# Kernel tuning notes

Hardware: AMD Instinct MI355X
Metric: run time of the kernel (lower is better)

The kernel has to match this reference:

```python
import jax, jax.numpy as jnp
import numpy as np

N_NODES = 20000
N_EDGES = 320000
NS = 16      # input scalar channels (0e)
NVH = 16     # hidden vector channels (1o)
STEPS = 3
BLOCKS = 2
SQRT3 = 3.0 ** 0.5  # component-normalized Y1


def _tp(xs, xv, ys, yv):
    """Tensor product of (0e,1o) features with (0e,1o) attrs, keeping 0e and 1o outputs.
    xs:[n,a] xv:[n,b,3] ys:[n,c] yv:[n,d,3] -> ts:[n,a*c+b*d], tv:[n,a*d+b*c,3]"""
    n = xs.shape[0]
    ss = jnp.einsum('na,nc->nac', xs, ys).reshape(n, -1)          # 0e x 0e -> 0e
    vv = jnp.einsum('nbi,ndi->nbd', xv, yv).reshape(n, -1)        # 1o . 1o -> 0e
    ts = jnp.concatenate([ss, vv], axis=-1)
    sv = jnp.einsum('na,ndi->nadi', xs, yv).reshape(n, -1, 3)     # 0e x 1o -> 1o
    vs = jnp.einsum('nbi,nc->nbci', xv, ys).reshape(n, -1, 3)     # 1o x 0e -> 1o
    tv = jnp.concatenate([sv, vs], axis=1)
    return ts, tv


def _tplg(xs, xv, ys, yv, Ws, bs, Wv, out_v):
    """TensorProductLinearGate: tensor product -> Linear -> gate (sigmoid gates on vectors, gelu on scalars)."""
    ts, tv = _tp(xs, xv, ys, yv)
    s = ts @ Ws + bs                                  # [n, out_v (gates) + out_s]
    v = jnp.einsum('npi,pq->nqi', tv, Wv)             # [n, out_v, 3]
    gates = jax.nn.sigmoid(s[:, :out_v])
    feat = jax.nn.gelu(s[:, out_v:])
    return feat, v * gates[:, :, None]


def _seg_mean(x, idx, n):
    s = jax.ops.segment_sum(x, idx, num_segments=n)
    cnt = jax.ops.segment_sum(jnp.ones((idx.shape[0],), x.dtype), idx, num_segments=n)
    return s / jnp.maximum(cnt, 1.0).reshape((n,) + (1,) * (x.ndim - 1))


def setup_inputs() -> dict:
    key = jax.random.key(0)
    ks = jax.random.split(key, 20)

    def w(k, shape):
        return jax.random.normal(k, shape, jnp.float32) / np.sqrt(shape[-2]).astype(np.float32)

    return {
        'node_scalars': jax.random.normal(ks[0], (N_NODES, NS), jnp.float32),
        'node_pos': jax.random.normal(ks[1], (N_NODES, 1, 3), jnp.float32),
        'senders': jax.random.randint(ks[2], (N_EDGES,), 0, N_NODES, jnp.int32),
        'receivers': jax.random.randint(ks[3], (N_EDGES,), 0, N_NODES, jnp.int32),
        'eWs0': w(ks[4], (STEPS, 34, 32)),
        'ebs0': jnp.zeros((STEPS, 32), jnp.float32),
        'eWv0': w(ks[5], (STEPS, 34, NVH)),
        'eWs1': w(ks[6], (STEPS, 32, 32)),
        'ebs1': jnp.zeros((STEPS, 32), jnp.float32),
        'eWv1': w(ks[7], (STEPS, 32, NVH)),
        'nWs': w(ks[8], (STEPS, BLOCKS, 289, 17)),
        'nbs': jnp.zeros((STEPS, BLOCKS, 17), jnp.float32),
        'nWv': w(ks[9], (STEPS, BLOCKS, 289, 1)),
        'fWs': w(ks[10], (STEPS, NS, NS)),
        'fbs': jnp.zeros((STEPS, NS), jnp.float32),
        'fWv': w(ks[11], (STEPS, 1, 1)),
    }


def reference(node_scalars, node_pos, senders, receivers, eWs0, ebs0, eWv0,
              eWs1, ebs1, eWv1, nWs, nbs, nWv, fWs, fbs, fWv):
    s, v = node_scalars, node_pos                      # [N,16], [N,1,3]
    N = s.shape[0]
    E = senders.shape[0]
    inv = 1.0 / (E - 1)                                # normalize_messages
    for t in range(STEPS):
        # --- edge update ---
        r = v[senders, 0] - v[receivers, 0]            # r_ij = x_i - x_j
        rhat = r / (jnp.linalg.norm(r, axis=-1, keepdims=True) + 1e-8)
        a_s = jnp.ones((E, 1), s.dtype)                # Y0 (component norm)
        a_v = (SQRT3 * rhat)[:, None, :]               # Y1 (component norm)
        xs = jnp.concatenate([s[senders], s[receivers]], axis=-1)
        xv = jnp.concatenate([v[senders], v[receivers]], axis=1)
        ms, mv = _tplg(xs, xv, a_s, a_v, eWs0[t], ebs0[t], eWv0[t], NVH)
        ms, mv = _tplg(ms, mv, a_s, a_v, eWs1[t], ebs1[t], eWv1[t], NVH)
        # --- aggregate (segment mean to receivers) + message normalization ---
        ys = jnp.concatenate([_seg_mean(ms, receivers, N), _seg_mean(a_s, receivers, N)], axis=-1) * inv
        yv = jnp.concatenate([_seg_mean(mv, receivers, N), _seg_mean(a_v, receivers, N)], axis=1) * inv
        # --- node update ---
        ns_, nv_ = s, v
        for b in range(BLOCKS):
            ns_, nv_ = _tplg(ns_, nv_, ys, yv, nWs[t, b], nbs[t, b], nWv[t, b], 1)
        # --- Linear back to irreps_in + residual ---
        s = s + ns_ @ fWs[t] + fbs[t]
        v = v + jnp.einsum('npi,pq->nqi', nv_, fWv[t])
    return jnp.concatenate([s, v.reshape(N, 3)], axis=-1)  # [N, 19]
```

## Files before the change

kernel.cpp:

```cpp
#include <hip/hip_runtime.h>

#define N_NODES 20000
#define N_EDGES 320000
#define CH 68

__device__ __forceinline__ float sigm(float x) { return 1.0f / (1.0f + __expf(-x)); }
__device__ __forceinline__ float gelu(float x) {
    return x * sigm(1.5957691216057308f * (x + 0.044715f * x * x * x));
}

__global__ void init_kernel(const float* __restrict__ s0, const float* __restrict__ p0,
                            float* __restrict__ s, float4* __restrict__ v4,
                            float* __restrict__ cnt) {
    int idx = blockIdx.x * 256 + threadIdx.x;
    if (idx < N_NODES * 16) s[idx] = s0[idx];
    if (idx < N_NODES) {
        v4[idx] = make_float4(p0[idx * 3], p0[idx * 3 + 1], p0[idx * 3 + 2], 0.f);
        cnt[idx] = 0.f;
    }
}

__global__ void count_kernel(const int* __restrict__ rcv, float* __restrict__ cnt) {
    int e = blockIdx.x * 256 + threadIdx.x;
    if (e < N_EDGES) unsafeAtomicAdd(&cnt[rcv[e]], 1.0f);
}

__global__ __launch_bounds__(1024) void scan_kernel(const float* __restrict__ cnt,
                                                    int* __restrict__ offs,
                                                    int* __restrict__ cursor) {
    __shared__ int sdata[1024];
    const int t = threadIdx.x;
    const int base = t * 20;
    int local[20];
    int sum = 0;
#pragma unroll
    for (int k = 0; k < 20; k++) {
        const int n = base + k;
        const int c = (n < N_NODES) ? (int)cnt[n] : 0;
        local[k] = sum;
        sum += c;
    }
    sdata[t] = sum;
    __syncthreads();
    for (int d = 1; d < 1024; d <<= 1) {
        const int v = (t >= d) ? sdata[t - d] : 0;
        __syncthreads();
        sdata[t] += v;
        __syncthreads();
    }
    const int pre = (t == 0) ? 0 : sdata[t - 1];
#pragma unroll
    for (int k = 0; k < 20; k++) {
        const int n = base + k;
        if (n < N_NODES) {
            offs[n] = pre + local[k];
            cursor[n] = 0;
        }
    }
}

__global__ void scatter_kernel(const int* __restrict__ rcv, const int* __restrict__ offs,
                               int* __restrict__ cursor, int* __restrict__ perm) {
    int e = blockIdx.x * 256 + threadIdx.x;
    if (e < N_EDGES) {
        const int n = rcv[e];
        const int slot = offs[n] + atomicAdd(&cursor[n], 1);
        perm[slot] = e;
    }
}

__global__ __launch_bounds__(256) void edge_compute_kernel(
    const float4* __restrict__ s4, const float4* __restrict__ v4,
    const int* __restrict__ snd, const int* __restrict__ rcv,
    const int* __restrict__ perm,
    const float* __restrict__ Ws0, const float* __restrict__ bs0, const float* __restrict__ Wv0,
    const float* __restrict__ Ws1, const float* __restrict__ bs1, const float* __restrict__ Wv1,
    float* __restrict__ msg) {
    __shared__ float lW[3168];
    const int tid = threadIdx.x;
    {
        for (int idx = tid; idx < 1088; idx += 256) lW[idx] = Ws0[idx];
        for (int idx = tid; idx < 544; idx += 256) lW[1088 + idx] = Wv0[idx];
        for (int idx = tid; idx < 1024; idx += 256) lW[1632 + idx] = Ws1[idx];
        for (int idx = tid; idx < 512; idx += 256) lW[2656 + idx] = Wv1[idx];
    }
    __syncthreads();
    const float* __restrict__ lWs0 = lW;
    const float* __restrict__ lWv0 = lW + 1088;
    const float* __restrict__ lWs1 = lW + 1632;
    const float* __restrict__ lWv1 = lW + 2656;

    const int e = blockIdx.x * 256 + tid;
    const int eid = perm[e];
    const int i = snd[eid], j = rcv[eid];

    const float4 vi4 = v4[i], vj4 = v4[j];
    const float vi0 = vi4.x, vi1 = vi4.y, vi2 = vi4.z;
    const float vj0 = vj4.x, vj1 = vj4.y, vj2 = vj4.z;
    const float r0 = vi0 - vj0, r1 = vi1 - vj1, r2 = vi2 - vj2;
    const float nrm = sqrtf(r0 * r0 + r1 * r1 + r2 * r2);
    const float scl = 1.7320508075688772f / (nrm + 1e-8f);
    const float a0 = r0 * scl, a1 = r1 * scl, a2 = r2 * scl;

    float xs[32];
    {
        float4 A = s4[i * 4 + 0], B = s4[i * 4 + 1], C = s4[i * 4 + 2], D = s4[i * 4 + 3];
        xs[0] = A.x; xs[1] = A.y; xs[2] = A.z; xs[3] = A.w;
        xs[4] = B.x; xs[5] = B.y; xs[6] = B.z; xs[7] = B.w;
        xs[8] = C.x; xs[9] = C.y; xs[10] = C.z; xs[11] = C.w;
        xs[12] = D.x; xs[13] = D.y; xs[14] = D.z; xs[15] = D.w;
        A = s4[j * 4 + 0]; B = s4[j * 4 + 1]; C = s4[j * 4 + 2]; D = s4[j * 4 + 3];
        xs[16] = A.x; xs[17] = A.y; xs[18] = A.z; xs[19] = A.w;
        xs[20] = B.x; xs[21] = B.y; xs[22] = B.z; xs[23] = B.w;
        xs[24] = C.x; xs[25] = C.y; xs[26] = C.z; xs[27] = C.w;
        xs[28] = D.x; xs[29] = D.y; xs[30] = D.z; xs[31] = D.w;
    }
    const float di = vi0 * a0 + vi1 * a1 + vi2 * a2;
    const float dj = vj0 * a0 + vj1 * a1 + vj2 * a2;

    float sl[32];
#pragma unroll
    for (int o = 0; o < 32; o++) sl[o] = bs0[o] + di * lWs0[32 * 32 + o] + dj * lWs0[33 * 32 + o];
#pragma unroll
    for (int p = 0; p < 32; p++) {
        const float x = xs[p];
#pragma unroll
        for (int o = 0; o < 32; o++) sl[o] += x * lWs0[p * 32 + o];
    }
    float al[16];
#pragma unroll
    for (int q = 0; q < 16; q++) al[q] = 0.f;
#pragma unroll
    for (int p = 0; p < 32; p++) {
        const float x = xs[p];
#pragma unroll
        for (int q = 0; q < 16; q++) al[q] += x * lWv0[p * 16 + q];
    }
    float ms[16], mv0[16], mv1[16], mv2[16];
#pragma unroll
    for (int q = 0; q < 16; q++) {
        const float g = sigm(sl[q]);
        const float w32 = lWv0[32 * 16 + q], w33 = lWv0[33 * 16 + q];
        mv0[q] = (al[q] * a0 + w32 * vi0 + w33 * vj0) * g;
        mv1[q] = (al[q] * a1 + w32 * vi1 + w33 * vj1) * g;
        mv2[q] = (al[q] * a2 + w32 * vi2 + w33 * vj2) * g;
    }
#pragma unroll
    for (int p = 0; p < 16; p++) ms[p] = gelu(sl[16 + p]);

    float sl2[32];
#pragma unroll
    for (int o = 0; o < 32; o++) sl2[o] = bs1[o];
#pragma unroll
    for (int p = 0; p < 16; p++) {
        const float x = ms[p];
#pragma unroll
        for (int o = 0; o < 32; o++) sl2[o] += x * lWs1[p * 32 + o];
    }
#pragma unroll
    for (int q = 0; q < 16; q++) {
        const float x = mv0[q] * a0 + mv1[q] * a1 + mv2[q] * a2;
#pragma unroll
        for (int o = 0; o < 32; o++) sl2[o] += x * lWs1[(16 + q) * 32 + o];
    }

    float4* mrow = (float4*)(msg + (size_t)e * CH);
    mrow[0] = make_float4(gelu(sl2[16]), gelu(sl2[17]), gelu(sl2[18]), gelu(sl2[19]));
    mrow[1] = make_float4(gelu(sl2[20]), gelu(sl2[21]), gelu(sl2[22]), gelu(sl2[23]));
    mrow[2] = make_float4(gelu(sl2[24]), gelu(sl2[25]), gelu(sl2[26]), gelu(sl2[27]));
    mrow[3] = make_float4(gelu(sl2[28]), gelu(sl2[29]), gelu(sl2[30]), gelu(sl2[31]));
#pragma unroll
    for (int qg = 0; qg < 4; qg++) {
        float t[12];
#pragma unroll
        for (int qq = 0; qq < 4; qq++) {
            const int q = qg * 4 + qq;
            const float g = sigm(sl2[q]);
            float be = 0.f;
#pragma unroll
            for (int p = 0; p < 16; p++) be += ms[p] * lWv1[p * 16 + q];
            float u0 = be * a0, u1 = be * a1, u2 = be * a2;
#pragma unroll
            for (int p = 0; p < 16; p++) {
                const float w = lWv1[(16 + p) * 16 + q];
                u0 += mv0[p] * w; u1 += mv1[p] * w; u2 += mv2[p] * w;
            }
            t[qq * 3 + 0] = u0 * g;
            t[qq * 3 + 1] = u1 * g;
            t[qq * 3 + 2] = u2 * g;
        }
        mrow[4 + qg * 3 + 0] = make_float4(t[0], t[1], t[2], t[3]);
        mrow[4 + qg * 3 + 1] = make_float4(t[4], t[5], t[6], t[7]);
        mrow[4 + qg * 3 + 2] = make_float4(t[8], t[9], t[10], t[11]);
    }
    mrow[16] = make_float4(a0, a1, a2, 0.f);
}

__global__ __launch_bounds__(256) void agg_kernel(const float* __restrict__ msg,
                                                  const float* __restrict__ cnt,
                                                  const int* __restrict__ offs,
                                                  float* __restrict__ agg) {
    const int id = blockIdx.x * 256 + threadIdx.x;
    if (id >= N_NODES * CH) return;
    const int n = id / CH;
    const int c = id - n * CH;
    const int deg = (int)cnt[n];
    const float* p = msg + (size_t)offs[n] * CH + c;
    float acc = 0.f;
    int r = 0;
    for (; r + 4 <= deg; r += 4) {
        acc += p[(size_t)(r + 0) * CH] + p[(size_t)(r + 1) * CH] +
               p[(size_t)(r + 2) * CH] + p[(size_t)(r + 3) * CH];
    }
    for (; r < deg; r++) acc += p[(size_t)r * CH];
    agg[id] = acc;
}

__global__ __launch_bounds__(256, 2) void node_kernel(
    float* __restrict__ s, float4* __restrict__ v4,
    float* __restrict__ agg, const float* __restrict__ cntb,
    const float* __restrict__ nWs, const float* __restrict__ nbs, const float* __restrict__ nWv,
    const float* __restrict__ fWs, const float* __restrict__ fbs, const float* __restrict__ fWv,
    float* __restrict__ out) {
    __shared__ float nsl[64 * 17];
    __shared__ float part[21 * 256];
    const int tid = threadIdx.x;
    const int lane = tid & 63;
    const int w = tid >> 6;
    const int n0 = blockIdx.x * 64 + lane;
    const bool valid = n0 < N_NODES;
    const int n = valid ? n0 : 0;
    const float inv = 1.0f / 319999.0f;
    const float cnt = cntb[n];
    const float f = inv / fmaxf(cnt, 1.0f);
    float* ag = agg + n * CH;
    const int c0 = w * 4;
    const bool w3 = (w == 3);

    float yso[4];
#pragma unroll
    for (int k = 0; k < 4; k++) yso[k] = ag[c0 + k] * f;
    const float ys16 = cnt * f;
    float yvo[4][3];
#pragma unroll
    for (int k = 0; k < 4; k++) {
        const int d = c0 + k;
        yvo[k][0] = ag[16 + d * 3 + 0] * f;
        yvo[k][1] = ag[16 + d * 3 + 1] * f;
        yvo[k][2] = ag[16 + d * 3 + 2] * f;
    }
    float yv16[3] = {ag[64] * f, ag[65] * f, ag[66] * f};
    const float4 nvv = v4[n];
    float nv0 = nvv.x, nv1 = nvv.y, nv2 = nvv.z;

    if (w == 0) {
        const float4* srow = (const float4*)(s + n * 16);
        const float4 A = srow[0], B = srow[1], C = srow[2], D = srow[3];
        float* p = nsl + lane * 17;
        p[0] = A.x; p[1] = A.y; p[2] = A.z; p[3] = A.w;
        p[4] = B.x; p[5] = B.y; p[6] = B.z; p[7] = B.w;
        p[8] = C.x; p[9] = C.y; p[10] = C.z; p[11] = C.w;
        p[12] = D.x; p[13] = D.y; p[14] = D.z; p[15] = D.w;
    }
    __syncthreads();

    float nsreg[16];
#pragma unroll 1
    for (int b = 0; b < 2; b++) {
        const float* W = nWs + b * 289 * 17;
        const float* Wv = nWv + b * 289;
        const float* bb = nbs + b * 17;
        float acc[17];
#pragma unroll
        for (int o = 0; o < 17; o++) acc[o] = (w == 0) ? bb[o] : 0.f;
        float gam[4] = {0.f, 0.f, 0.f, 0.f};
        float gam16 = 0.f;
#pragma unroll 2
        for (int a = 0; a < 16; a++) {
            const float xa = nsl[lane * 17 + a];
            const float* Wa = W + (a * 17 + c0) * 17;
#pragma unroll
            for (int k = 0; k < 4; k++) {
                const float cf = xa * yso[k];
#pragma unroll
                for (int o = 0; o < 17; o++) acc[o] += cf * Wa[k * 17 + o];
            }
            const float* Wva = Wv + a * 17 + c0;
#pragma unroll
            for (int k = 0; k < 4; k++) gam[k] += xa * Wva[k];
            if (w3) {
                const float cf = xa * ys16;
                const float* W16 = W + (a * 17 + 16) * 17;
#pragma unroll
                for (int o = 0; o < 17; o++) acc[o] += cf * W16[o];
                gam16 += xa * Wv[a * 17 + 16];
            }
        }
#pragma unroll
        for (int k = 0; k < 4; k++) {
            const int d = c0 + k;
            const float cf = nv0 * yvo[k][0] + nv1 * yvo[k][1] + nv2 * yvo[k][2];
            const float* Wp = W + (272 + d) * 17;
#pragma unroll
            for (int o = 0; o < 17; o++) acc[o] += cf * Wp[o];
        }
        if (w3) {
            const float cf = nv0 * yv16[0] + nv1 * yv16[1] + nv2 * yv16[2];
            const float* Wp = W + (272 + 16) * 17;
#pragma unroll
            for (int o = 0; o < 17; o++) acc[o] += cf * Wp[o];
        }
        float vl0 = 0.f, vl1 = 0.f, vl2 = 0.f, sc2 = 0.f;
#pragma unroll
        for (int k = 0; k < 4; k++) {
            vl0 += gam[k] * yvo[k][0]; vl1 += gam[k] * yvo[k][1]; vl2 += gam[k] * yvo[k][2];
            sc2 += yso[k] * Wv[272 + c0 + k];
        }
        if (w3) {
            vl0 += gam16 * yv16[0]; vl1 += gam16 * yv16[1]; vl2 += gam16 * yv16[2];
            sc2 += ys16 * Wv[272 + 16];
        }
#pragma unroll
        for (int o = 0; o < 17; o++) part[o * 256 + tid] = acc[o];
        part[17 * 256 + tid] = vl0;
        part[18 * 256 + tid] = vl1;
        part[19 * 256 + tid] = vl2;
        part[20 * 256 + tid] = sc2;
        __syncthreads();
        float tot[21];
#pragma unroll
        for (int t = 0; t < 21; t++)
            tot[t] = part[t * 256 + lane] + part[t * 256 + 64 + lane] +
                     part[t * 256 + 128 + lane] + part[t * 256 + 192 + lane];
        const float g = sigm(tot[0]);
#pragma unroll
        for (int a = 0; a < 16; a++) nsreg[a] = gelu(tot[1 + a]);
        const float nx = (tot[17] + tot[20] * nv0) * g;
        const float ny = (tot[18] + tot[20] * nv1) * g;
        const float nz = (tot[19] + tot[20] * nv2) * g;
        nv0 = nx; nv1 = ny; nv2 = nz;
        if (b == 0 && w == 0) {
            float* p = nsl + lane * 17;
#pragma unroll
            for (int a = 0; a < 16; a++) p[a] = nsreg[a];
        }
        __syncthreads();
    }
    float so[16];
#pragma unroll
    for (int a = 0; a < 16; a++) so[a] = fbs[a];
#pragma unroll
    for (int p = 0; p < 16; p++) {
        const float x = nsreg[p];
#pragma unroll
        for (int a = 0; a < 16; a++) so[a] += x * fWs[p * 16 + a];
    }
    if (valid && w == 0) {
        const float fw = fWv[0];
        float sn[16];
#pragma unroll
        for (int a = 0; a < 16; a++) { sn[a] = s[n * 16 + a] + so[a]; }
#pragma unroll
        for (int a = 0; a < 16; a++) s[n * 16 + a] = sn[a];
        const float w0o = nvv.x + nv0 * fw;
        const float w1o = nvv.y + nv1 * fw;
        const float w2o = nvv.z + nv2 * fw;
        v4[n] = make_float4(w0o, w1o, w2o, 0.f);
        if (out) {
#pragma unroll
            for (int a = 0; a < 16; a++) out[n * 19 + a] = sn[a];
            out[n * 19 + 16] = w0o;
            out[n * 19 + 17] = w1o;
            out[n * 19 + 18] = w2o;
        }
    }
}

extern "C" void kernel_launch(void* const* d_in, const int* in_sizes, int n_in,
                              void* d_out, int out_size, void* d_ws, size_t ws_size,
                              hipStream_t stream) {
    const float* node_scalars = (const float*)d_in[0];
    const float* node_pos = (const float*)d_in[1];
    const int* senders = (const int*)d_in[2];
    const int* receivers = (const int*)d_in[3];
    const float* eWs0 = (const float*)d_in[4];
    const float* ebs0 = (const float*)d_in[5];
    const float* eWv0 = (const float*)d_in[6];
    const float* eWs1 = (const float*)d_in[7];
    const float* ebs1 = (const float*)d_in[8];
    const float* eWv1 = (const float*)d_in[9];
    const float* nWs = (const float*)d_in[10];
    const float* nbs = (const float*)d_in[11];
    const float* nWv = (const float*)d_in[12];
    const float* fWs = (const float*)d_in[13];
    const float* fbs = (const float*)d_in[14];
    const float* fWv = (const float*)d_in[15];

    float* ws = (float*)d_ws;
    float* s = ws;
    float* v = s + N_NODES * 16;
    float* agg = v + N_NODES * 4;
    float* cnt = agg + N_NODES * CH;
    int* offs = (int*)(cnt + N_NODES);
    int* cursor = offs + N_NODES;
    int* perm = cursor + N_NODES;
    float* msg = (float*)(perm + N_EDGES);
    float* out = (float*)d_out;
    float4* v4 = (float4*)v;

    init_kernel<<<(N_NODES * 16 + 255) / 256, 256, 0, stream>>>(node_scalars, node_pos, s, v4, cnt);
    count_kernel<<<(N_EDGES + 255) / 256, 256, 0, stream>>>(receivers, cnt);
    scan_kernel<<<1, 1024, 0, stream>>>(cnt, offs, cursor);
    scatter_kernel<<<(N_EDGES + 255) / 256, 256, 0, stream>>>(receivers, offs, cursor, perm);
    for (int t = 0; t < 3; t++) {
        edge_compute_kernel<<<N_EDGES / 256, 256, 0, stream>>>(
            (const float4*)s, (const float4*)v4, senders, receivers, perm,
            eWs0 + t * 34 * 32, ebs0 + t * 32, eWv0 + t * 34 * 16,
            eWs1 + t * 32 * 32, ebs1 + t * 32, eWv1 + t * 32 * 16,
            msg);
        agg_kernel<<<(N_NODES * CH + 255) / 256, 256, 0, stream>>>(msg, cnt, offs, agg);
        node_kernel<<<(N_NODES + 63) / 64, 256, 0, stream>>>(
            s, v4, agg, cnt,
            nWs + t * 2 * 289 * 17, nbs + t * 2 * 17, nWv + t * 2 * 289,
            fWs + t * 256, fbs + t * 16, fWv + t,
            (t == 2) ? out : nullptr);
    }
}
```

Baseline: 629.2 us.

## Process two edges per thread in edge kernel and stage node weights in LDS

Each thread of the edge kernel now computes two edges, so every weight value read from shared memory feeds two FMAs. This halves the grid and the per-block weight staging, with launch bounds set to allow two blocks per CU. The node kernel now copies each block's weight matrix and the final linear weights into shared memory instead of reading them from global memory. The cost is higher register pressure in the edge kernel, which may cause spills or lower occupancy, plus extra LDS and a sync per block in the node kernel.

```diff
diff --git a/kernel.cpp b/kernel.cpp
--- a/kernel.cpp
+++ b/kernel.cpp
@@ -69,7 +69,7 @@
     }
 }
 
-__global__ __launch_bounds__(256) void edge_compute_kernel(
+__global__ __launch_bounds__(256, 2) void edge_compute_kernel(
     const float4* __restrict__ s4, const float4* __restrict__ v4,
     const int* __restrict__ snd, const int* __restrict__ rcv,
     const int* __restrict__ perm,
@@ -90,110 +90,169 @@
     const float* __restrict__ lWs1 = lW + 1632;
     const float* __restrict__ lWv1 = lW + 2656;
 
-    const int e = blockIdx.x * 256 + tid;
-    const int eid = perm[e];
-    const int i = snd[eid], j = rcv[eid];
-
-    const float4 vi4 = v4[i], vj4 = v4[j];
-    const float vi0 = vi4.x, vi1 = vi4.y, vi2 = vi4.z;
-    const float vj0 = vj4.x, vj1 = vj4.y, vj2 = vj4.z;
-    const float r0 = vi0 - vj0, r1 = vi1 - vj1, r2 = vi2 - vj2;
-    const float nrm = sqrtf(r0 * r0 + r1 * r1 + r2 * r2);
-    const float scl = 1.7320508075688772f / (nrm + 1e-8f);
-    const float a0 = r0 * scl, a1 = r1 * scl, a2 = r2 * scl;
-
-    float xs[32];
+    const int eA = blockIdx.x * 512 + tid;
+    const int eB = eA + 256;
+    const int eidA = perm[eA], eidB = perm[eB];
+    const int iA = snd[eidA], jA = rcv[eidA];
+    const int iB = snd[eidB], jB = rcv[eidB];
+
+    const float4 viA4 = v4[iA], vjA4 = v4[jA];
+    const float4 viB4 = v4[iB], vjB4 = v4[jB];
+    const float vi0A = viA4.x, vi1A = viA4.y, vi2A = viA4.z;
+    const float vj0A = vjA4.x, vj1A = vjA4.y, vj2A = vjA4.z;
+    const float vi0B = viB4.x, vi1B = viB4.y, vi2B = viB4.z;
+    const float vj0B = vjB4.x, vj1B = vjB4.y, vj2B = vjB4.z;
+    float a0A, a1A, a2A, a0B, a1B, a2B;
     {
-        float4 A = s4[i * 4 + 0], B = s4[i * 4 + 1], C = s4[i * 4 + 2], D = s4[i * 4 + 3];
-        xs[0] = A.x; xs[1] = A.y; xs[2] = A.z; xs[3] = A.w;
-        xs[4] = B.x; xs[5] = B.y; xs[6] = B.z; xs[7] = B.w;
-        xs[8] = C.x; xs[9] = C.y; xs[10] = C.z; xs[11] = C.w;
-        xs[12] = D.x; xs[13] = D.y; xs[14] = D.z; xs[15] = D.w;
-        A = s4[j * 4 + 0]; B = s4[j * 4 + 1]; C = s4[j * 4 + 2]; D = s4[j * 4 + 3];
-        xs[16] = A.x; xs[17] = A.y; xs[18] = A.z; xs[19] = A.w;
-        xs[20] = B.x; xs[21] = B.y; xs[22] = B.z; xs[23] = B.w;
-        xs[24] = C.x; xs[25] = C.y; xs[26] = C.z; xs[27] = C.w;
-        xs[28] = D.x; xs[29] = D.y; xs[30] = D.z; xs[31] = D.w;
-    }
-    const float di = vi0 * a0 + vi1 * a1 + vi2 * a2;
-    const float dj = vj0 * a0 + vj1 * a1 + vj2 * a2;
-
-    float sl[32];
-#pragma unroll
-    for (int o = 0; o < 32; o++) sl[o] = bs0[o] + di * lWs0[32 * 32 + o] + dj * lWs0[33 * 32 + o];
+        const float r0 = vi0A - vj0A, r1 = vi1A - vj1A, r2 = vi2A - vj2A;
+        const float scl = 1.7320508075688772f / (sqrtf(r0 * r0 + r1 * r1 + r2 * r2) + 1e-8f);
+        a0A = r0 * scl; a1A = r1 * scl; a2A = r2 * scl;
+    }
+    {
+        const float r0 = vi0B - vj0B, r1 = vi1B - vj1B, r2 = vi2B - vj2B;
+        const float scl = 1.7320508075688772f / (sqrtf(r0 * r0 + r1 * r1 + r2 * r2) + 1e-8f);
+        a0B = r0 * scl; a1B = r1 * scl; a2B = r2 * scl;
+    }
+
+    float xsA[32], xsB[32];
+    {
+        float4 A = s4[iA * 4 + 0], B = s4[iA * 4 + 1], C = s4[iA * 4 + 2], D = s4[iA * 4 + 3];
+        xsA[0] = A.x; xsA[1] = A.y; xsA[2] = A.z; xsA[3] = A.w;
+        xsA[4] = B.x; xsA[5] = B.y; xsA[6] = B.z; xsA[7] = B.w;
+        xsA[8] = C.x; xsA[9] = C.y; xsA[10] = C.z; xsA[11] = C.w;
+        xsA[12] = D.x; xsA[13] = D.y; xsA[14] = D.z; xsA[15] = D.w;
+        A = s4[jA * 4 + 0]; B = s4[jA * 4 + 1]; C = s4[jA * 4 + 2]; D = s4[jA * 4 + 3];
+        xsA[16] = A.x; xsA[17] = A.y; xsA[18] = A.z; xsA[19] = A.w;
+        xsA[20] = B.x; xsA[21] = B.y; xsA[22] = B.z; xsA[23] = B.w;
+        xsA[24] = C.x; xsA[25] = C.y; xsA[26] = C.z; xsA[27] = C.w;
+        xsA[28] = D.x; xsA[29] = D.y; xsA[30] = D.z; xsA[31] = D.w;
+        A = s4[iB * 4 + 0]; B = s4[iB * 4 + 1]; C = s4[iB * 4 + 2]; D = s4[iB * 4 + 3];
+        xsB[0] = A.x; xsB[1] = A.y; xsB[2] = A.z; xsB[3] = A.w;
+        xsB[4] = B.x; xsB[5] = B.y; xsB[6] = B.z; xsB[7] = B.w;
+        xsB[8] = C.x; xsB[9] = C.y; xsB[10] = C.z; xsB[11] = C.w;
+        xsB[12] = D.x; xsB[13] = D.y; xsB[14] = D.z; xsB[15] = D.w;
+        A = s4[jB * 4 + 0]; B = s4[jB * 4 + 1]; C = s4[jB * 4 + 2]; D = s4[jB * 4 + 3];
+        xsB[16] = A.x; xsB[17] = A.y; xsB[18] = A.z; xsB[19] = A.w;
+        xsB[20] = B.x; xsB[21] = B.y; xsB[22] = B.z; xsB[23] = B.w;
+        xsB[24] = C.x; xsB[25] = C.y; xsB[26] = C.z; xsB[27] = C.w;
+        xsB[28] = D.x; xsB[29] = D.y; xsB[30] = D.z; xsB[31] = D.w;
+    }
+    const float diA = vi0A * a0A + vi1A * a1A + vi2A * a2A;
+    const float djA = vj0A * a0A + vj1A * a1A + vj2A * a2A;
+    const float diB = vi0B * a0B + vi1B * a1B + vi2B * a2B;
+    const float djB = vj0B * a0B + vj1B * a1B + vj2B * a2B;
+
+    float slA[32], slB[32];
+#pragma unroll
+    for (int o = 0; o < 32; o++) {
+        const float b = bs0[o], w32 = lWs0[1024 + o], w33 = lWs0[1056 + o];
+        slA[o] = b + diA * w32 + djA * w33;
+        slB[o] = b + diB * w32 + djB * w33;
+    }
 #pragma unroll
     for (int p = 0; p < 32; p++) {
-        const float x = xs[p];
-#pragma unroll
-        for (int o = 0; o < 32; o++) sl[o] += x * lWs0[p * 32 + o];
-    }
-    float al[16];
-#pragma unroll
-    for (int q = 0; q < 16; q++) al[q] = 0.f;
+        const float xA = xsA[p], xB = xsB[p];
+#pragma unroll
+        for (int o = 0; o < 32; o++) {
+            const float w = lWs0[p * 32 + o];
+            slA[o] += xA * w; slB[o] += xB * w;
+        }
+    }
+    float alA[16], alB[16];
+#pragma unroll
+    for (int q = 0; q < 16; q++) { alA[q] = 0.f; alB[q] = 0.f; }
 #pragma unroll
     for (int p = 0; p < 32; p++) {
-        const float x = xs[p];
-#pragma unroll
-        for (int q = 0; q < 16; q++) al[q] += x * lWv0[p * 16 + q];
-    }
-    float ms[16], mv0[16], mv1[16], mv2[16];
+        const float xA = xsA[p], xB = xsB[p];
+#pragma unroll
+        for (int q = 0; q < 16; q++) {
+            const float w = lWv0[p * 16 + q];
+            alA[q] += xA * w; alB[q] += xB * w;
+        }
+    }
+    float msA[16], mv0A[16], mv1A[16], mv2A[16];
+    float msB[16], mv0B[16], mv1B[16], mv2B[16];
 #pragma unroll
     for (int q = 0; q < 16; q++) {
-        const float g = sigm(sl[q]);
-        const float w32 = lWv0[32 * 16 + q], w33 = lWv0[33 * 16 + q];
-        mv0[q] = (al[q] * a0 + w32 * vi0 + w33 * vj0) * g;
-        mv1[q] = (al[q] * a1 + w32 * vi1 + w33 * vj1) * g;
-        mv2[q] = (al[q] * a2 + w32 * vi2 + w33 * vj2) * g;
-    }
-#pragma unroll
-    for (int p = 0; p < 16; p++) ms[p] = gelu(sl[16 + p]);
-
-    float sl2[32];
-#pragma unroll
-    for (int o = 0; o < 32; o++) sl2[o] = bs1[o];
+        const float w32 = lWv0[512 + q], w33 = lWv0[528 + q];
+        const float gA = sigm(slA[q]);
+        mv0A[q] = (alA[q] * a0A + w32 * vi0A + w33 * vj0A) * gA;
+        mv1A[q] = (alA[q] * a1A + w32 * vi1A + w33 * vj1A) * gA;
+        mv2A[q] = (alA[q] * a2A + w32 * vi2A + w33 * vj2A) * gA;
+        const float gB = sigm(slB[q]);
+        mv0B[q] = (alB[q] * a0B + w32 * vi0B + w33 * vj0B) * gB;
+        mv1B[q] = (alB[q] * a1B + w32 * vi1B + w33 * vj1B) * gB;
+        mv2B[q] = (alB[q] * a2B + w32 * vi2B + w33 * vj2B) * gB;
+    }
+#pragma unroll
+    for (int p = 0; p < 16; p++) { msA[p] = gelu(slA[16 + p]); msB[p] = gelu(slB[16 + p]); }
+
+    float sl2A[32], sl2B[32];
+#pragma unroll
+    for (int o = 0; o < 32; o++) { const float b = bs1[o]; sl2A[o] = b; sl2B[o] = b; }
 #pragma unroll
     for (int p = 0; p < 16; p++) {
-        const float x = ms[p];
-#pragma unroll
-        for (int o = 0; o < 32; o++) sl2[o] += x * lWs1[p * 32 + o];
+        const float xA = msA[p], xB = msB[p];
+#pragma unroll
+        for (int o = 0; o < 32; o++) {
+            const float w = lWs1[p * 32 + o];
+            sl2A[o] += xA * w; sl2B[o] += xB * w;
+        }
     }
 #pragma unroll
     for (int q = 0; q < 16; q++) {
-        const float x = mv0[q] * a0 + mv1[q] * a1 + mv2[q] * a2;
-#pragma unroll
-        for (int o = 0; o < 32; o++) sl2[o] += x * lWs1[(16 + q) * 32 + o];
-    }
-
-    float4* mrow = (float4*)(msg + (size_t)e * CH);
-    mrow[0] = make_float4(gelu(sl2[16]), gelu(sl2[17]), gelu(sl2[18]), gelu(sl2[19]));
-    mrow[1] = make_float4(gelu(sl2[20]), gelu(sl2[21]), gelu(sl2[22]), gelu(sl2[23]));
-    mrow[2] = make_float4(gelu(sl2[24]), gelu(sl2[25]), gelu(sl2[26]), gelu(sl2[27]));
-    mrow[3] = make_float4(gelu(sl2[28]), gelu(sl2[29]), gelu(sl2[30]), gelu(sl2[31]));
+        const float xA = mv0A[q] * a0A + mv1A[q] * a1A + mv2A[q] * a2A;
+        const float xB = mv0B[q] * a0B + mv1B[q] * a1B + mv2B[q] * a2B;
+#pragma unroll
+        for (int o = 0; o < 32; o++) {
+            const float w = lWs1[(16 + q) * 32 + o];
+            sl2A[o] += xA * w; sl2B[o] += xB * w;
+        }
+    }
+
+    float4* mrowA = (float4*)(msg + (size_t)eA * CH);
+    float4* mrowB = (float4*)(msg + (size_t)eB * CH);
+    mrowA[0] = make_float4(gelu(sl2A[16]), gelu(sl2A[17]), gelu(sl2A[18]), gelu(sl2A[19]));
+    mrowA[1] = make_float4(gelu(sl2A[20]), gelu(sl2A[21]), gelu(sl2A[22]), gelu(sl2A[23]));
+    mrowA[2] = make_float4(gelu(sl2A[24]), gelu(sl2A[25]), gelu(sl2A[26]), gelu(sl2A[27]));
+    mrowA[3] = make_float4(gelu(sl2A[28]), gelu(sl2A[29]), gelu(sl2A[30]), gelu(sl2A[31]));
+    mrowB[0] = make_float4(gelu(sl2B[16]), gelu(sl2B[17]), gelu(sl2B[18]), gelu(sl2B[19]));
+    mrowB[1] = make_float4(gelu(sl2B[20]), gelu(sl2B[21]), gelu(sl2B[22]), gelu(sl2B[23]));
+    mrowB[2] = make_float4(gelu(sl2B[24]), gelu(sl2B[25]), gelu(sl2B[26]), gelu(sl2B[27]));
+    mrowB[3] = make_float4(gelu(sl2B[28]), gelu(sl2B[29]), gelu(sl2B[30]), gelu(sl2B[31]));
 #pragma unroll
     for (int qg = 0; qg < 4; qg++) {
-        float t[12];
+        float tA[12], tB[12];
 #pragma unroll
         for (int qq = 0; qq < 4; qq++) {
             const int q = qg * 4 + qq;
-            const float g = sigm(sl2[q]);
-            float be = 0.f;
-#pragma unroll
-            for (int p = 0; p < 16; p++) be += ms[p] * lWv1[p * 16 + q];
-            float u0 = be * a0, u1 = be * a1, u2 = be * a2;
+            float beA = 0.f, beB = 0.f;
+#pragma unroll
+            for (int p = 0; p < 16; p++) {
+                const float w = lWv1[p * 16 + q];
+                beA += msA[p] * w; beB += msB[p] * w;
+            }
+            float u0A = beA * a0A, u1A = beA * a1A, u2A = beA * a2A;
+            float u0B = beB * a0B, u1B = beB * a1B, u2B = beB * a2B;
 #pragma unroll
             for (int p = 0; p < 16; p++) {
                 const float w = lWv1[(16 + p) * 16 + q];
-                u0 += mv0[p] * w; u1 += mv1[p] * w; u2 += mv2[p] * w;
+                u0A += mv0A[p] * w; u1A += mv1A[p] * w; u2A += mv2A[p] * w;
+                u0B += mv0B[p] * w; u1B += mv1B[p] * w; u2B += mv2B[p] * w;
             }
-            t[qq * 3 + 0] = u0 * g;
-            t[qq * 3 + 1] = u1 * g;
-            t[qq * 3 + 2] = u2 * g;
-        }
-        mrow[4 + qg * 3 + 0] = make_float4(t[0], t[1], t[2], t[3]);
-        mrow[4 + qg * 3 + 1] = make_float4(t[4], t[5], t[6], t[7]);
-        mrow[4 + qg * 3 + 2] = make_float4(t[8], t[9], t[10], t[11]);
-    }
-    mrow[16] = make_float4(a0, a1, a2, 0.f);
+            const float gA = sigm(sl2A[q]), gB = sigm(sl2B[q]);
+            tA[qq * 3 + 0] = u0A * gA; tA[qq * 3 + 1] = u1A * gA; tA[qq * 3 + 2] = u2A * gA;
+            tB[qq * 3 + 0] = u0B * gB; tB[qq * 3 + 1] = u1B * gB; tB[qq * 3 + 2] = u2B * gB;
+        }
+        mrowA[4 + qg * 3 + 0] = make_float4(tA[0], tA[1], tA[2], tA[3]);
+        mrowA[4 + qg * 3 + 1] = make_float4(tA[4], tA[5], tA[6], tA[7]);
+        mrowA[4 + qg * 3 + 2] = make_float4(tA[8], tA[9], tA[10], tA[11]);
+        mrowB[4 + qg * 3 + 0] = make_float4(tB[0], tB[1], tB[2], tB[3]);
+        mrowB[4 + qg * 3 + 1] = make_float4(tB[4], tB[5], tB[6], tB[7]);
+        mrowB[4 + qg * 3 + 2] = make_float4(tB[8], tB[9], tB[10], tB[11]);
+    }
+    mrowA[16] = make_float4(a0A, a1A, a2A, 0.f);
+    mrowB[16] = make_float4(a0B, a1B, a2B, 0.f);
 }
 
 __global__ __launch_bounds__(256) void agg_kernel(const float* __restrict__ msg,
@@ -224,6 +283,8 @@
     float* __restrict__ out) {
     __shared__ float nsl[64 * 17];
     __shared__ float part[21 * 256];
+    __shared__ float lw[289 * 17 + 289];
+    __shared__ float lf[256];
     const int tid = threadIdx.x;
     const int lane = tid & 63;
     const int w = tid >> 6;
@@ -237,6 +298,8 @@
     const int c0 = w * 4;
     const bool w3 = (w == 3);
 
+    if (tid < 256) lf[tid] = fWs[tid];
+
     float yso[4];
 #pragma unroll
     for (int k = 0; k < 4; k++) yso[k] = ag[c0 + k] * f;
@@ -262,13 +325,15 @@
         p[8] = C.x; p[9] = C.y; p[10] = C.z; p[11] = C.w;
         p[12] = D.x; p[13] = D.y; p[14] = D.z; p[15] = D.w;
     }
-    __syncthreads();
 
     float nsreg[16];
 #pragma unroll 1
     for (int b = 0; b < 2; b++) {
-        const float* W = nWs + b * 289 * 17;
-        const float* Wv = nWv + b * 289;
+        for (int idx = tid; idx < 289 * 17; idx += 256) lw[idx] = nWs[b * 289 * 17 + idx];
+        for (int idx = tid; idx < 289; idx += 256) lw[289 * 17 + idx] = nWv[b * 289 + idx];
+        __syncthreads();
+        const float* W = lw;
+        const float* Wv = lw + 289 * 17;
         const float* bb = nbs + b * 17;
         float acc[17];
 #pragma unroll
@@ -353,7 +418,7 @@
     for (int p = 0; p < 16; p++) {
         const float x = nsreg[p];
 #pragma unroll
-        for (int a = 0; a < 16; a++) so[a] += x * fWs[p * 16 + a];
+        for (int a = 0; a < 16; a++) so[a] += x * lf[p * 16 + a];
     }
     if (valid && w == 0) {
         const float fw = fWv[0];
@@ -413,7 +478,7 @@
     scan_kernel<<<1, 1024, 0, stream>>>(cnt, offs, cursor);
     scatter_kernel<<<(N_EDGES + 255) / 256, 256, 0, stream>>>(receivers, offs, cursor, perm);
     for (int t = 0; t < 3; t++) {
-        edge_compute_kernel<<<N_EDGES / 256, 256, 0, stream>>>(
+        edge_compute_kernel<<<N_EDGES / 512, 256, 0, stream>>>(
             (const float4*)s, (const float4*)v4, senders, receivers, perm,
             eWs0 + t * 34 * 32, ebs0 + t * 32, eWv0 + t * 34 * 16,
             eWs1 + t * 32 * 32, ebs1 + t * 32, eWv1 + t * 32 * 16,
```

Result: slower. 920.0 us (+46.2%).

## Fuse segment aggregation into node kernel and stage node weights in LDS

Applied to the files above, without the earlier changes.

Removes the separate aggregation kernel: each node block now sums its receiver-sorted message rows itself, four threads per node using float4 loads, and writes the 68-channel sums to shared memory, so the agg buffer is never written to or read back from global memory. The node weight matrices for each block, and fWs, are also copied into LDS rather than read from global memory inside the inner loops. The costs are much more LDS per block (about 40KB), which may lower occupancy, and a serial per-node reduction loop whose length follows node degree, which can cause imbalance between threads.

```diff
diff --git a/kernel.cpp b/kernel.cpp
--- a/kernel.cpp
+++ b/kernel.cpp
@@ -196,34 +196,17 @@
     mrow[16] = make_float4(a0, a1, a2, 0.f);
 }
 
-__global__ __launch_bounds__(256) void agg_kernel(const float* __restrict__ msg,
-                                                  const float* __restrict__ cnt,
-                                                  const int* __restrict__ offs,
-                                                  float* __restrict__ agg) {
-    const int id = blockIdx.x * 256 + threadIdx.x;
-    if (id >= N_NODES * CH) return;
-    const int n = id / CH;
-    const int c = id - n * CH;
-    const int deg = (int)cnt[n];
-    const float* p = msg + (size_t)offs[n] * CH + c;
-    float acc = 0.f;
-    int r = 0;
-    for (; r + 4 <= deg; r += 4) {
-        acc += p[(size_t)(r + 0) * CH] + p[(size_t)(r + 1) * CH] +
-               p[(size_t)(r + 2) * CH] + p[(size_t)(r + 3) * CH];
-    }
-    for (; r < deg; r++) acc += p[(size_t)r * CH];
-    agg[id] = acc;
-}
-
 __global__ __launch_bounds__(256, 2) void node_kernel(
     float* __restrict__ s, float4* __restrict__ v4,
-    float* __restrict__ agg, const float* __restrict__ cntb,
+    const float* __restrict__ msg, const int* __restrict__ offs,
+    const float* __restrict__ cntb,
     const float* __restrict__ nWs, const float* __restrict__ nbs, const float* __restrict__ nWv,
     const float* __restrict__ fWs, const float* __restrict__ fbs, const float* __restrict__ fWv,
     float* __restrict__ out) {
     __shared__ float nsl[64 * 17];
-    __shared__ float part[21 * 256];
+    __shared__ float u[21 * 256];
+    __shared__ float lw[289 * 17 + 289];
+    __shared__ float lf[256];
     const int tid = threadIdx.x;
     const int lane = tid & 63;
     const int w = tid >> 6;
@@ -231,9 +214,45 @@
     const bool valid = n0 < N_NODES;
     const int n = valid ? n0 : 0;
     const float inv = 1.0f / 319999.0f;
+
+    if (tid < 256) lf[tid] = fWs[tid];
+
+    {
+        const int nl = tid >> 2;
+        const int q = tid & 3;
+        const int gn0 = blockIdx.x * 64 + nl;
+        const int gn = (gn0 < N_NODES) ? gn0 : 0;
+        const int o0 = offs[gn];
+        const int deg = (gn0 < N_NODES) ? (int)cntb[gn] : 0;
+        float4 acc0 = make_float4(0.f, 0.f, 0.f, 0.f);
+        float4 acc1 = acc0, acc2 = acc0, acc3 = acc0, acc4 = acc0;
+        for (int r = 0; r < deg; r++) {
+            const float4* row = (const float4*)(msg + (size_t)(o0 + r) * CH);
+            const float4 t0 = row[q];
+            const float4 t1 = row[q + 4];
+            const float4 t2 = row[q + 8];
+            const float4 t3 = row[q + 12];
+            acc0.x += t0.x; acc0.y += t0.y; acc0.z += t0.z; acc0.w += t0.w;
+            acc1.x += t1.x; acc1.y += t1.y; acc1.z += t1.z; acc1.w += t1.w;
+            acc2.x += t2.x; acc2.y += t2.y; acc2.z += t2.z; acc2.w += t2.w;
+            acc3.x += t3.x; acc3.y += t3.y; acc3.z += t3.z; acc3.w += t3.w;
+            if (q == 0) {
+                const float4 t4 = row[16];
+                acc4.x += t4.x; acc4.y += t4.y; acc4.z += t4.z; acc4.w += t4.w;
+            }
+        }
+        float4* rowl = (float4*)(u + nl * CH);
+        rowl[q] = acc0;
+        rowl[q + 4] = acc1;
+        rowl[q + 8] = acc2;
+        rowl[q + 12] = acc3;
+        if (q == 0) rowl[16] = acc4;
+    }
+    __syncthreads();
+
     const float cnt = cntb[n];
     const float f = inv / fmaxf(cnt, 1.0f);
-    float* ag = agg + n * CH;
+    const float* ag = u + lane * CH;
     const int c0 = w * 4;
     const bool w3 = (w == 3);
 
@@ -262,14 +281,17 @@
         p[8] = C.x; p[9] = C.y; p[10] = C.z; p[11] = C.w;
         p[12] = D.x; p[13] = D.y; p[14] = D.z; p[15] = D.w;
     }
-    __syncthreads();
 
     float nsreg[16];
 #pragma unroll 1
     for (int b = 0; b < 2; b++) {
-        const float* W = nWs + b * 289 * 17;
-        const float* Wv = nWv + b * 289;
+        for (int idx = tid; idx < 289 * 17; idx += 256) lw[idx] = nWs[b * 289 * 17 + idx];
+        for (int idx = tid; idx < 289; idx += 256) lw[289 * 17 + idx] = nWv[b * 289 + idx];
+        __syncthreads();
+        const float* W = lw;
+        const float* Wv = lw + 289 * 17;
         const float* bb = nbs + b * 17;
+        float* part = u;
         float acc[17];
 #pragma unroll
         for (int o = 0; o < 17; o++) acc[o] = (w == 0) ? bb[o] : 0.f;
@@ -353,7 +375,7 @@
     for (int p = 0; p < 16; p++) {
         const float x = nsreg[p];
 #pragma unroll
-        for (int a = 0; a < 16; a++) so[a] += x * fWs[p * 16 + a];
+        for (int a = 0; a < 16; a++) so[a] += x * lf[p * 16 + a];
     }
     if (valid && w == 0) {
         const float fw = fWv[0];
@@ -399,8 +421,7 @@
     float* ws = (float*)d_ws;
     float* s = ws;
     float* v = s + N_NODES * 16;
-    float* agg = v + N_NODES * 4;
-    float* cnt = agg + N_NODES * CH;
+    float* cnt = v + N_NODES * 4;
     int* offs = (int*)(cnt + N_NODES);
     int* cursor = offs + N_NODES;
     int* perm = cursor + N_NODES;
@@ -418,9 +439,8 @@
             eWs0 + t * 34 * 32, ebs0 + t * 32, eWv0 + t * 34 * 16,
             eWs1 + t * 32 * 32, ebs1 + t * 32, eWv1 + t * 32 * 16,
             msg);
-        agg_kernel<<<(N_NODES * CH + 255) / 256, 256, 0, stream>>>(msg, cnt, offs, agg);
         node_kernel<<<(N_NODES + 63) / 64, 256, 0, stream>>>(
-            s, v4, agg, cnt,
+            s, v4, msg, offs, cnt,
             nWs + t * 2 * 289 * 17, nbs + t * 2 * 17, nWv + t * 2 * 289,
             fWs + t * 256, fbs + t * 16, fWv + t,
             (t == 2) ? out : nullptr);
```

Measured after the change: 581.0 us (median of 2 runs). 1.08x faster.
